# Kernel tuning notes

Measured on AMD Instinct MI355X. Metric: run time of the kernel, lower is better.

## Reference

```python
import jax, jax.numpy as jnp
import numpy as np

ALPHA = 5.0
LAMBDA = 1.0


def setup_inputs() -> dict:
    key = jax.random.key(0)
    k1, k2 = jax.random.split(key)
    N, BITS, NCLASS = 2048, 64, 32
    b = jax.random.normal(k1, (N, BITS), dtype=jnp.float32)
    y = jax.random.randint(k2, (N,), 0, NCLASS, dtype=jnp.int32)
    return {"b": b, "y": y}


def reference(b, y):
    # similarity = 0.5 * <b_i, b_j>  -> [N, N]
    sim = 0.5 * (b @ b.T)
    # affinity: same-label pairs (equivalent to onehot(y) @ onehot(y).T > 0)
    aff = y[:, None] == y[None, :]  # [N, N] bool
    N = sim.shape[0]

    def step(carry, i):
        loss_sum, cnt = carry
        pos = aff[i]            # [N] bool, positives for row i
        theta = sim[i]          # [N]
        # triple[p, n] = theta_pos[p] - theta_neg[n] - alpha, clamped
        t = jnp.clip(theta[:, None] - theta[None, :] - ALPHA, -100.0, 50.0)
        # -(t - log(1 + exp(t))) == log1p(exp(t)) - t  (== softplus(-t))
        val = jnp.log1p(jnp.exp(t)) - t
        mask = pos[:, None] & (~pos)[None, :]
        npairs = mask.sum()
        valid = pos.any() & (~pos).any()
        row_loss = jnp.where(
            valid,
            jnp.where(mask, val, 0.0).sum() / jnp.maximum(npairs, 1).astype(val.dtype),
            0.0,
        )
        return (loss_sum + row_loss, cnt + valid.astype(jnp.float32)), None

    init = (jnp.float32(0.0), jnp.float32(0.0))
    (loss_sum, cnt), _ = jax.lax.scan(step, init, jnp.arange(N))
    loss1 = jnp.where(cnt > 0, loss_sum / jnp.maximum(cnt, 1.0), 0.0)
    # quantization loss (sign has zero gradient, same as torch)
    loss2 = jnp.mean((b - jnp.sign(b)) ** 2)
    total = loss1 + LAMBDA * loss2
    return total, loss1, loss2
```

## Files before the change

### kernel.cpp

```cpp
#include <hip/hip_runtime.h>
#include <math.h>

#define NROW 2048
#define BITS 64
#define MB 512
#define RPB 4
#define JQ 4
#define NBLK (NROW / RPB)
#define NWV (MB / 64)
#define MAXPOS 256

#define LN2_F   0.6931471805599453f
#define THSCALE 0.7213475204444817f
#define A_SC    7.213475204444817f

__global__ __launch_bounds__(256) void bt_kernel(const float* __restrict__ b,
                                                 float* __restrict__ bT)
{
    __shared__ float tile[64][65];
    const int t  = threadIdx.x;
    const int j0 = blockIdx.x * 64;
    {
        const int jj = t >> 2, q = t & 3;
        const float4* b4 = reinterpret_cast<const float4*>(b + (size_t)(j0 + jj) * BITS);
#pragma unroll
        for (int m = 0; m < 4; ++m) {
            const float4 v = b4[q * 4 + m];
            const int col = q * 16 + m * 4;
            tile[jj][col + 0] = v.x; tile[jj][col + 1] = v.y;
            tile[jj][col + 2] = v.z; tile[jj][col + 3] = v.w;
        }
    }
    __syncthreads();
    {
        const int k = t >> 2, q = t & 3;
#pragma unroll
        for (int s = 0; s < 4; ++s) {
            float4 v;
            v.x = tile[q * 16 + s * 4 + 0][k];
            v.y = tile[q * 16 + s * 4 + 1][k];
            v.z = tile[q * 16 + s * 4 + 2][k];
            v.w = tile[q * 16 + s * 4 + 3][k];
            *reinterpret_cast<float4*>(&bT[(size_t)k * NROW + j0 + q * 16 + s * 4]) = v;
        }
    }
}

template <bool TR>
__global__ __launch_bounds__(MB) void dhn_main(
    const float* __restrict__ b, const float* __restrict__ bT,
    const int* __restrict__ y,
    float* __restrict__ blockLoss, float* __restrict__ blockValid,
    float* __restrict__ blockQ)
{
    const int br  = blockIdx.x;
    const int i0  = br * RPB;
    const int tid = threadIdx.x;
    const int w = tid >> 6, lane = tid & 63;

    __shared__ __align__(16) float  biT[BITS * RPB];
    __shared__ __align__(16) float  posPe[RPB][MAXPOS + 8];
    __shared__ __align__(16) float4 posSG[RPB][MAXPOS / 4 + 2];
    __shared__ int   waveTot[RPB][NWV];
    __shared__ int   waveBase[RPB][NWV];
    __shared__ int   pcnt[RPB];
    __shared__ float wred[NWV], wq[NWV];

    if (tid < BITS * RPB) {
        const int k = tid >> 2, r = tid & 3;
        biT[tid] = b[(size_t)(i0 + r) * BITS + k];
    }
    __syncthreads();

    float th[JQ][RPB] = {};
    if constexpr (TR) {
        const float4* bt4 = reinterpret_cast<const float4*>(bT);
        const float4* bi4 = reinterpret_cast<const float4*>(biT);
#pragma unroll 8
        for (int k = 0; k < BITS; ++k) {
            const float4 bj = bt4[k * (NROW / 4) + tid];
            const float4 bi = bi4[k];
            th[0][0] += bj.x * bi.x; th[0][1] += bj.x * bi.y;
            th[0][2] += bj.x * bi.z; th[0][3] += bj.x * bi.w;
            th[1][0] += bj.y * bi.x; th[1][1] += bj.y * bi.y;
            th[1][2] += bj.y * bi.z; th[1][3] += bj.y * bi.w;
            th[2][0] += bj.z * bi.x; th[2][1] += bj.z * bi.y;
            th[2][2] += bj.z * bi.z; th[2][3] += bj.z * bi.w;
            th[3][0] += bj.w * bi.x; th[3][1] += bj.w * bi.y;
            th[3][2] += bj.w * bi.z; th[3][3] += bj.w * bi.w;
        }
    } else {
        for (int k = 0; k < BITS; ++k) {
#pragma unroll
            for (int q = 0; q < JQ; ++q) {
                const float v = b[(size_t)(4 * tid + q) * BITS + k];
#pragma unroll
                for (int r = 0; r < RPB; ++r) th[q][r] += v * biT[k * 4 + r];
            }
        }
    }

    const int4 y4 = reinterpret_cast<const int4*>(y)[tid];
    const int yj[JQ] = { y4.x, y4.y, y4.z, y4.w };
    int yr[RPB];
#pragma unroll
    for (int r = 0; r < RPB; ++r) yr[r] = y[i0 + r];

    float ev[JQ][RPB];
    int pm[RPB], cnt[RPB];
#pragma unroll
    for (int r = 0; r < RPB; ++r) {
        int m = 0;
#pragma unroll
        for (int q = 0; q < JQ; ++q) {
            const float t2 = th[q][r] * THSCALE;
            const bool f = (yj[q] == yr[r]);
            ev[q][r] = __builtin_amdgcn_exp2f(f ? -t2 : t2 + A_SC);
            if (f) m |= 1 << q;
        }
        pm[r] = m;
        cnt[r] = __popc(m);
    }

    int excl[RPB];
#pragma unroll
    for (int r = 0; r < RPB; ++r) {
        int v = cnt[r];
#pragma unroll
        for (int off = 1; off < 64; off <<= 1) {
            const int t2 = __shfl_up(v, off);
            if (lane >= off) v += t2;
        }
        excl[r] = v - cnt[r];
        if (lane == 63) waveTot[r][w] = v;
    }
    __syncthreads();
    if (tid < RPB) {
        int base = 0;
#pragma unroll
        for (int wv = 0; wv < NWV; ++wv) { waveBase[tid][wv] = base; base += waveTot[tid][wv]; }
        pcnt[tid] = base;
    }
    __syncthreads();

#pragma unroll
    for (int r = 0; r < RPB; ++r) {
        int o = waveBase[r][w] + excl[r];
#pragma unroll
        for (int q = 0; q < JQ; ++q) {
            if ((pm[r] >> q) & 1) {
                if (o < MAXPOS) posPe[r][o] = ev[q][r];
                ++o;
            }
        }
    }
    if (tid < RPB * 8) {
        const int r = tid >> 3, q = tid & 7;
        const int P = pcnt[r] < MAXPOS ? pcnt[r] : MAXPOS;
        const int idx = P + q;
        if (idx < ((P + 7) & ~7)) posPe[r][idx] = 0.f;
    }
    __syncthreads();

    if (tid < RPB * (MAXPOS / 4)) {
        const int r = tid / (MAXPOS / 4);
        const int g = tid % (MAXPOS / 4);
        const int P = pcnt[r] < MAXPOS ? pcnt[r] : MAXPOS;
        const int Ppad = (P + 7) & ~7;
        if (g * 4 < Ppad) {
            float c1 = 0.f, c2 = 0.f, c3 = 0.f, c4 = 0.f;
#pragma unroll
            for (int k = 0; k < 4; ++k) {
                const float p = posPe[r][g * 4 + k];
                c4 = fmaf(p, c3, c4);
                c3 = fmaf(p, c2, c3);
                c2 = fmaf(p, c1, c2);
                c1 += p;
            }
            posSG[r][g] = make_float4(c1, c2, c3, c4);
        }
    }
    __syncthreads();

    float total = 0.f;
#pragma unroll
    for (int r = 0; r < RPB; ++r) {
        const int Pc = pcnt[r];
        const int P  = Pc < MAXPOS ? Pc : MAXPOS;
        const int PG = ((P + 7) & ~7) >> 3;
        float e[JQ];
#pragma unroll
        for (int q = 0; q < JQ; ++q)
            e[q] = ((pm[r] >> q) & 1) ? 0.f : ev[q][r];
        float a[JQ] = {};
        const float4* sg4 = &posSG[r][0];
        for (int g = 0; g < PG; ++g) {
            const float4 A = sg4[2 * g + 0];
            const float4 B = sg4[2 * g + 1];
#pragma unroll
            for (int q = 0; q < JQ; ++q) {
                const float eq = e[q];
                const float hA = fmaf(fmaf(fmaf(fmaf(A.w, eq, A.z), eq, A.y), eq, A.x), eq, 1.f);
                const float hB = fmaf(fmaf(fmaf(fmaf(B.w, eq, B.z), eq, B.y), eq, B.x), eq, 1.f);
                a[q] += __builtin_amdgcn_logf(hA) + __builtin_amdgcn_logf(hB);
            }
        }
#pragma unroll
        for (int q = 0; q < JQ; ++q) {
            if (__builtin_expect(isinf(a[q]), 0)) {
                const float eq = e[q];
                float s = 0.f;
                for (int p = 0; p < P; ++p)
                    s += __builtin_amdgcn_logf(fmaf(eq, posPe[r][p], 1.f));
                a[q] = s;
            }
        }
        const bool valid = (Pc > 0) && (Pc < NROW);
        const float denom = (float)Pc * (float)(NROW - Pc);
        total += valid ? ((a[0] + a[1]) + (a[2] + a[3])) / denom : 0.f;
    }
    total *= LN2_F;

    float q2 = 0.f;
    if (tid < BITS * RPB) {
        const float x  = biT[tid];
        const float sg = (x > 0.f) ? 1.f : ((x < 0.f) ? -1.f : 0.f);
        const float d  = x - sg;
        q2 = d * d;
    }

#pragma unroll
    for (int off = 32; off > 0; off >>= 1) {
        total += __shfl_xor(total, off);
        q2    += __shfl_xor(q2, off);
    }
    if (lane == 0) { wred[w] = total; wq[w] = q2; }
    __syncthreads();
    if (tid == 0) {
        float tl = 0.f, tq = 0.f;
#pragma unroll
        for (int v = 0; v < NWV; ++v) { tl += wred[v]; tq += wq[v]; }
        blockLoss[br] = tl;
        blockQ[br]    = tq;
        float vc = 0.f;
#pragma unroll
        for (int r = 0; r < RPB; ++r)
            vc += ((pcnt[r] > 0) && (pcnt[r] < NROW)) ? 1.f : 0.f;
        blockValid[br] = vc;
    }
}

__global__ __launch_bounds__(256) void dhn_final_kernel(
    const float* __restrict__ blockLoss, const float* __restrict__ blockValid,
    const float* __restrict__ blockQ, float* __restrict__ out)
{
    const int tid = threadIdx.x;
    const int w = tid >> 6, lane = tid & 63;
    __shared__ float r1[4], r2[4], r3[4];

    float sl = 0.f, sv = 0.f, sq = 0.f;
    for (int i = tid; i < NBLK; i += 256) {
        sl += blockLoss[i]; sv += blockValid[i]; sq += blockQ[i];
    }
#pragma unroll
    for (int off = 32; off > 0; off >>= 1) {
        sl += __shfl_xor(sl, off);
        sv += __shfl_xor(sv, off);
        sq += __shfl_xor(sq, off);
    }
    if (lane == 0) { r1[w] = sl; r2[w] = sv; r3[w] = sq; }
    __syncthreads();
    if (tid == 0) {
        float SL = 0.f, SV = 0.f, SQ = 0.f;
#pragma unroll
        for (int v = 0; v < 4; ++v) { SL += r1[v]; SV += r2[v]; SQ += r3[v]; }
        const float loss1 = (SV > 0.f) ? SL / fmaxf(SV, 1.f) : 0.f;
        const float loss2 = SQ / (float)(NROW * BITS);
        out[0] = loss1 + 1.0f * loss2;
        out[1] = loss1;
        out[2] = loss2;
    }
}

extern "C" void kernel_launch(void* const* d_in, const int* in_sizes, int n_in,
                              void* d_out, int out_size, void* d_ws, size_t ws_size,
                              hipStream_t stream) {
    const float* b = (const float*)d_in[0];
    const int*   y = (const int*)d_in[1];
    float* out = (float*)d_out;

    float* blockLoss  = (float*)d_ws;
    float* blockValid = (float*)((char*)d_ws + 4096);
    float* blockQ     = (float*)((char*)d_ws + 8192);
    float* bT         = (float*)((char*)d_ws + 16384);

    const size_t need = 16384 + (size_t)BITS * NROW * sizeof(float);
    if (ws_size >= need) {
        bt_kernel<<<NROW / 64, 256, 0, stream>>>(b, bT);
        dhn_main<true><<<NBLK, MB, 0, stream>>>(b, bT, y, blockLoss, blockValid, blockQ);
    } else {
        dhn_main<false><<<NBLK, MB, 0, stream>>>(b, nullptr, y, blockLoss, blockValid, blockQ);
    }
    dhn_final_kernel<<<1, 256, 0, stream>>>(blockLoss, blockValid, blockQ, out);
}
```

Measured before the change: 43.67 us.

## Precompute per-row positive sets and prefix sums in a prep kernel

```diff
diff --git a/kernel.cpp b/kernel.cpp
--- a/kernel.cpp
+++ b/kernel.cpp
@@ -8,48 +8,103 @@
 #define JQ 4
 #define NBLK (NROW / RPB)
 #define NWV (MB / 64)
-#define MAXPOS 256
+#define MAXPOS 128
 
 #define LN2_F   0.6931471805599453f
 #define THSCALE 0.7213475204444817f
 #define A_SC    7.213475204444817f
 
-__global__ __launch_bounds__(256) void bt_kernel(const float* __restrict__ b,
-                                                 float* __restrict__ bT)
+__global__ __launch_bounds__(256) void prep_kernel(
+    const float* __restrict__ b, const int* __restrict__ y,
+    float* __restrict__ bT, float4* __restrict__ posSGg,
+    float* __restrict__ posPeG, int* __restrict__ pcntG)
 {
-    __shared__ float tile[64][65];
-    const int t  = threadIdx.x;
-    const int j0 = blockIdx.x * 64;
-    {
-        const int jj = t >> 2, q = t & 3;
-        const float4* b4 = reinterpret_cast<const float4*>(b + (size_t)(j0 + jj) * BITS);
-#pragma unroll
-        for (int m = 0; m < 4; ++m) {
-            const float4 v = b4[q * 4 + m];
-            const int col = q * 16 + m * 4;
-            tile[jj][col + 0] = v.x; tile[jj][col + 1] = v.y;
-            tile[jj][col + 2] = v.z; tile[jj][col + 3] = v.w;
-        }
-    }
-    __syncthreads();
-    {
-        const int k = t >> 2, q = t & 3;
-#pragma unroll
-        for (int s = 0; s < 4; ++s) {
-            float4 v;
-            v.x = tile[q * 16 + s * 4 + 0][k];
-            v.y = tile[q * 16 + s * 4 + 1][k];
-            v.z = tile[q * 16 + s * 4 + 2][k];
-            v.w = tile[q * 16 + s * 4 + 3][k];
-            *reinterpret_cast<float4*>(&bT[(size_t)k * NROW + j0 + q * 16 + s * 4]) = v;
-        }
-    }
-}
-
-template <bool TR>
+    const int t = threadIdx.x;
+    if (blockIdx.x < 32) {
+        __shared__ float tile[64][65];
+        const int j0 = blockIdx.x * 64;
+        {
+            const int jj = t >> 2, q = t & 3;
+            const float4* b4 = reinterpret_cast<const float4*>(b + (size_t)(j0 + jj) * BITS);
+#pragma unroll
+            for (int m = 0; m < 4; ++m) {
+                const float4 v = b4[q * 4 + m];
+                const int col = q * 16 + m * 4;
+                tile[jj][col + 0] = v.x; tile[jj][col + 1] = v.y;
+                tile[jj][col + 2] = v.z; tile[jj][col + 3] = v.w;
+            }
+        }
+        __syncthreads();
+        {
+            const int k = t >> 2, q = t & 3;
+#pragma unroll
+            for (int s = 0; s < 4; ++s) {
+                float4 v;
+                v.x = tile[q * 16 + s * 4 + 0][k];
+                v.y = tile[q * 16 + s * 4 + 1][k];
+                v.z = tile[q * 16 + s * 4 + 2][k];
+                v.w = tile[q * 16 + s * 4 + 3][k];
+                *reinterpret_cast<float4*>(&bT[(size_t)k * NROW + j0 + q * 16 + s * 4]) = v;
+            }
+        }
+        return;
+    }
+
+    const int w = t >> 6, lane = t & 63;
+    const int i = (blockIdx.x - 32) * 4 + w;
+    __shared__ float biS[4][BITS];
+    __shared__ float peS[4][MAXPOS];
+
+    biS[w][lane] = b[(size_t)i * BITS + lane];
+    peS[w][lane] = 0.f;
+    peS[w][lane + 64] = 0.f;
+
+    const int yi = y[i];
+    const unsigned long long lm = (1ull << lane) - 1ull;
+    const float4* bi4 = reinterpret_cast<const float4*>(&biS[w][0]);
+    int base = 0;
+    for (int c = 0; c < NROW / 64; ++c) {
+        const int j = c * 64 + lane;
+        const bool f = (y[j] == yi);
+        const unsigned long long mp = __ballot(f);
+        if (f) {
+            const float4* rp = reinterpret_cast<const float4*>(b + (size_t)j * BITS);
+            float acc = 0.f;
+#pragma unroll
+            for (int k4 = 0; k4 < BITS / 4; ++k4) {
+                const float4 a = bi4[k4], v = rp[k4];
+                acc += a.x * v.x + a.y * v.y + a.z * v.z + a.w * v.w;
+            }
+            const int idx = base + (int)__popcll(mp & lm);
+            if (idx < MAXPOS) peS[w][idx] = __builtin_amdgcn_exp2f(-THSCALE * acc);
+        }
+        base += (int)__popcll(mp);
+    }
+    if (lane == 0) pcntG[i] = base;
+
+    posPeG[(size_t)i * MAXPOS + lane]      = peS[w][lane];
+    posPeG[(size_t)i * MAXPOS + 64 + lane] = peS[w][lane + 64];
+
+    if (lane < MAXPOS / 4) {
+        float c1 = 0.f, c2 = 0.f, c3 = 0.f, c4 = 0.f;
+#pragma unroll
+        for (int k = 0; k < 4; ++k) {
+            const float p = peS[w][lane * 4 + k];
+            c4 = fmaf(p, c3, c4);
+            c3 = fmaf(p, c2, c3);
+            c2 = fmaf(p, c1, c2);
+            c1 += p;
+        }
+        posSGg[(size_t)i * (MAXPOS / 4) + lane] = make_float4(c1, c2, c3, c4);
+    }
+}
+
+template <bool WS>
 __global__ __launch_bounds__(MB) void dhn_main(
     const float* __restrict__ b, const float* __restrict__ bT,
     const int* __restrict__ y,
+    const float4* __restrict__ posSGg, const float* __restrict__ posPeG,
+    const int* __restrict__ pcntG,
     float* __restrict__ blockLoss, float* __restrict__ blockValid,
     float* __restrict__ blockQ)
 {
@@ -58,12 +113,7 @@
     const int tid = threadIdx.x;
     const int w = tid >> 6, lane = tid & 63;
 
-    __shared__ __align__(16) float  biT[BITS * RPB];
-    __shared__ __align__(16) float  posPe[RPB][MAXPOS + 8];
-    __shared__ __align__(16) float4 posSG[RPB][MAXPOS / 4 + 2];
-    __shared__ int   waveTot[RPB][NWV];
-    __shared__ int   waveBase[RPB][NWV];
-    __shared__ int   pcnt[RPB];
+    __shared__ __align__(16) float biT[BITS * RPB];
     __shared__ float wred[NWV], wq[NWV];
 
     if (tid < BITS * RPB) {
@@ -73,7 +123,7 @@
     __syncthreads();
 
     float th[JQ][RPB] = {};
-    if constexpr (TR) {
+    if constexpr (WS) {
         const float4* bt4 = reinterpret_cast<const float4*>(bT);
         const float4* bi4 = reinterpret_cast<const float4*>(biT);
 #pragma unroll 8
@@ -102,98 +152,22 @@
 
     const int4 y4 = reinterpret_cast<const int4*>(y)[tid];
     const int yj[JQ] = { y4.x, y4.y, y4.z, y4.w };
-    int yr[RPB];
-#pragma unroll
-    for (int r = 0; r < RPB; ++r) yr[r] = y[i0 + r];
-
-    float ev[JQ][RPB];
-    int pm[RPB], cnt[RPB];
+
+    float total = 0.f;
 #pragma unroll
     for (int r = 0; r < RPB; ++r) {
-        int m = 0;
-#pragma unroll
-        for (int q = 0; q < JQ; ++q) {
-            const float t2 = th[q][r] * THSCALE;
-            const bool f = (yj[q] == yr[r]);
-            ev[q][r] = __builtin_amdgcn_exp2f(f ? -t2 : t2 + A_SC);
-            if (f) m |= 1 << q;
-        }
-        pm[r] = m;
-        cnt[r] = __popc(m);
-    }
-
-    int excl[RPB];
-#pragma unroll
-    for (int r = 0; r < RPB; ++r) {
-        int v = cnt[r];
-#pragma unroll
-        for (int off = 1; off < 64; off <<= 1) {
-            const int t2 = __shfl_up(v, off);
-            if (lane >= off) v += t2;
-        }
-        excl[r] = v - cnt[r];
-        if (lane == 63) waveTot[r][w] = v;
-    }
-    __syncthreads();
-    if (tid < RPB) {
-        int base = 0;
-#pragma unroll
-        for (int wv = 0; wv < NWV; ++wv) { waveBase[tid][wv] = base; base += waveTot[tid][wv]; }
-        pcnt[tid] = base;
-    }
-    __syncthreads();
-
-#pragma unroll
-    for (int r = 0; r < RPB; ++r) {
-        int o = waveBase[r][w] + excl[r];
-#pragma unroll
-        for (int q = 0; q < JQ; ++q) {
-            if ((pm[r] >> q) & 1) {
-                if (o < MAXPOS) posPe[r][o] = ev[q][r];
-                ++o;
-            }
-        }
-    }
-    if (tid < RPB * 8) {
-        const int r = tid >> 3, q = tid & 7;
-        const int P = pcnt[r] < MAXPOS ? pcnt[r] : MAXPOS;
-        const int idx = P + q;
-        if (idx < ((P + 7) & ~7)) posPe[r][idx] = 0.f;
-    }
-    __syncthreads();
-
-    if (tid < RPB * (MAXPOS / 4)) {
-        const int r = tid / (MAXPOS / 4);
-        const int g = tid % (MAXPOS / 4);
-        const int P = pcnt[r] < MAXPOS ? pcnt[r] : MAXPOS;
-        const int Ppad = (P + 7) & ~7;
-        if (g * 4 < Ppad) {
-            float c1 = 0.f, c2 = 0.f, c3 = 0.f, c4 = 0.f;
-#pragma unroll
-            for (int k = 0; k < 4; ++k) {
-                const float p = posPe[r][g * 4 + k];
-                c4 = fmaf(p, c3, c4);
-                c3 = fmaf(p, c2, c3);
-                c2 = fmaf(p, c1, c2);
-                c1 += p;
-            }
-            posSG[r][g] = make_float4(c1, c2, c3, c4);
-        }
-    }
-    __syncthreads();
-
-    float total = 0.f;
-#pragma unroll
-    for (int r = 0; r < RPB; ++r) {
-        const int Pc = pcnt[r];
+        const int yr = y[i0 + r];
+        const int Pc = pcntG[i0 + r];
         const int P  = Pc < MAXPOS ? Pc : MAXPOS;
         const int PG = ((P + 7) & ~7) >> 3;
         float e[JQ];
 #pragma unroll
-        for (int q = 0; q < JQ; ++q)
-            e[q] = ((pm[r] >> q) & 1) ? 0.f : ev[q][r];
+        for (int q = 0; q < JQ; ++q) {
+            const float t2 = th[q][r] * THSCALE + A_SC;
+            e[q] = (yj[q] == yr) ? 0.f : __builtin_amdgcn_exp2f(t2);
+        }
         float a[JQ] = {};
-        const float4* sg4 = &posSG[r][0];
+        const float4* sg4 = posSGg + (size_t)(i0 + r) * (MAXPOS / 4);
         for (int g = 0; g < PG; ++g) {
             const float4 A = sg4[2 * g + 0];
             const float4 B = sg4[2 * g + 1];
@@ -211,13 +185,14 @@
                 const float eq = e[q];
                 float s = 0.f;
                 for (int p = 0; p < P; ++p)
-                    s += __builtin_amdgcn_logf(fmaf(eq, posPe[r][p], 1.f));
+                    s += __builtin_amdgcn_logf(fmaf(eq, posPeG[(size_t)(i0 + r) * MAXPOS + p], 1.f));
                 a[q] = s;
             }
         }
-        const bool valid = (Pc > 0) && (Pc < NROW);
-        const float denom = (float)Pc * (float)(NROW - Pc);
-        total += valid ? ((a[0] + a[1]) + (a[2] + a[3])) / denom : 0.f;
+        if ((Pc > 0) && (Pc < NROW)) {
+            const float denom = (float)Pc * (float)(NROW - Pc);
+            total += ((a[0] + a[1]) + (a[2] + a[3])) / denom;
+        }
     }
     total *= LN2_F;
 
@@ -244,8 +219,10 @@
         blockQ[br]    = tq;
         float vc = 0.f;
 #pragma unroll
-        for (int r = 0; r < RPB; ++r)
-            vc += ((pcnt[r] > 0) && (pcnt[r] < NROW)) ? 1.f : 0.f;
+        for (int r = 0; r < RPB; ++r) {
+            const int P = pcntG[i0 + r];
+            vc += ((P > 0) && (P < NROW)) ? 1.f : 0.f;
+        }
         blockValid[br] = vc;
     }
 }
@@ -289,17 +266,24 @@
     const int*   y = (const int*)d_in[1];
     float* out = (float*)d_out;
 
-    float* blockLoss  = (float*)d_ws;
-    float* blockValid = (float*)((char*)d_ws + 4096);
-    float* blockQ     = (float*)((char*)d_ws + 8192);
-    float* bT         = (float*)((char*)d_ws + 16384);
-
-    const size_t need = 16384 + (size_t)BITS * NROW * sizeof(float);
+    float*  blockLoss  = (float*)d_ws;
+    float*  blockValid = (float*)((char*)d_ws + 4096);
+    float*  blockQ     = (float*)((char*)d_ws + 8192);
+    int*    pcntG      = (int*)((char*)d_ws + 12288);
+    float*  bT         = (float*)((char*)d_ws + 24576);
+    float4* posSGg     = (float4*)((char*)d_ws + 24576 + 524288);
+    float*  posPeG     = (float*)((char*)d_ws + 24576 + 524288 + 1048576);
+
+    const size_t need = 24576 + 524288 + 1048576 + (size_t)NROW * MAXPOS * sizeof(float);
     if (ws_size >= need) {
-        bt_kernel<<<NROW / 64, 256, 0, stream>>>(b, bT);
-        dhn_main<true><<<NBLK, MB, 0, stream>>>(b, bT, y, blockLoss, blockValid, blockQ);
+        prep_kernel<<<32 + NROW / 4, 256, 0, stream>>>(b, y, bT, posSGg, posPeG, pcntG);
+        dhn_main<true><<<NBLK, MB, 0, stream>>>(b, bT, y, posSGg, posPeG, pcntG,
+                                                blockLoss, blockValid, blockQ);
+        dhn_final_kernel<<<1, 256, 0, stream>>>(blockLoss, blockValid, blockQ, out);
     } else {
-        dhn_main<false><<<NBLK, MB, 0, stream>>>(b, nullptr, y, blockLoss, blockValid, blockQ);
-    }
-    dhn_final_kernel<<<1, 256, 0, stream>>>(blockLoss, blockValid, blockQ, out);
-}
+        prep_kernel<<<32 + NROW / 4, 256, 0, stream>>>(b, y, bT, posSGg, posPeG, pcntG);
+        dhn_main<false><<<NBLK, MB, 0, stream>>>(b, nullptr, y, posSGg, posPeG, pcntG,
+                                                 blockLoss, blockValid, blockQ);
+        dhn_final_kernel<<<1, 256, 0, stream>>>(blockLoss, blockValid, blockQ, out);
+    }
+}
```

Result: slower. 77.29 us (+77.0%).
